# Optimization experiments

Hardware: AMD Instinct MI355X
Metric: run time of the kernel (lower is better)

## Reference

```python
import jax, jax.numpy as jnp
import numpy as np

N_NODE, N_USER = 100000, 30000
N_REL, N_BASIS = 8, 30
EMB, OUT = 32, 32
E = 1600000
BATCH = 16384
H1, H2, H3 = 64, 32, 16
NEG_SLOPE = 0.2


def setup_inputs() -> dict:
    key = jax.random.key(0)
    ks = jax.random.split(key, 20)
    g = lambda k, shape: jax.random.normal(k, shape, dtype=jnp.float32) * 0.05
    inp = {
        "x_ids": jnp.arange(N_NODE, dtype=jnp.int64 if jax.config.jax_enable_x64 else jnp.int32),
        "edge_index": jax.random.randint(ks[0], (2, E), 0, N_NODE),
        "edge_type": jax.random.randint(ks[1], (E,), 0, N_REL),
        "users": jax.random.randint(ks[2], (BATCH,), 0, N_USER),
        "bundles": jax.random.randint(ks[3], (BATCH,), 0, N_NODE),
        # parameters
        "emb": g(ks[4], (N_NODE, EMB)),
        "basis": g(ks[5], (N_BASIS, EMB, OUT)),
        "weight": g(ks[6], (N_REL, N_BASIS)),
        "att": g(ks[7], (N_REL, 2 * OUT)),
        "root": g(ks[8], (EMB, OUT)),
        "bias": jnp.zeros((OUT,), jnp.float32),
        "W1": g(ks[9], (2 * OUT, H1)), "b1": jnp.zeros((H1,), jnp.float32),
        "W2": g(ks[10], (H1, H2)), "b2": jnp.zeros((H2,), jnp.float32),
        "W3": g(ks[11], (H2, H3)), "b3": jnp.zeros((H3,), jnp.float32),
        "Wo": g(ks[12], (H3, 1)), "bo": jnp.zeros((1,), jnp.float32),
    }
    return inp


def _tgcn_fwd(x_ids, edge_index, edge_type, users, bundles,
              emb, basis, weight, att, root, bias,
              W1, b1, W2, b2, W3, b3, Wo, bo):
    N = emb.shape[0]
    R = weight.shape[0]
    O = basis.shape[2]
    x = emb[x_ids]                                   # (N, F) embedding lookup
    # basis decomposition: (R, F, O)
    w = (weight @ basis.reshape(N_BASIS, -1)).reshape(R, EMB, O)
    # transform every node under every relation once, then gather per edge
    xh = jnp.einsum('nf,rfo->nro', x, w)             # (N, R, O)
    src, dst = edge_index[0], edge_index[1]          # j (source), i (target)
    h_i = xh[dst, edge_type]                         # (E, O)
    h_j = xh[src, edge_type]                         # (E, O)
    a = att[edge_type]                               # (E, 2O)
    alpha = (h_i * a[:, :O]).sum(-1) + (h_j * a[:, O:]).sum(-1)
    alpha = jax.nn.leaky_relu(alpha, NEG_SLOPE)
    # segment softmax keyed by (target node, relation)
    seg_key = dst * R + edge_type
    n_seg = N * R
    amax = jax.ops.segment_max(alpha, seg_key, num_segments=n_seg)
    ex = jnp.exp(alpha - amax[seg_key])
    denom = jax.ops.segment_sum(ex, seg_key, num_segments=n_seg)
    alpha = ex / (denom[seg_key] + 1e-16)
    # scatter-add weighted messages into target nodes
    agg = jax.ops.segment_sum(h_j * alpha[:, None], dst, num_segments=N)
    h = jax.nn.relu(agg + x @ root + bias)           # update + ReLU
    z = jnp.concatenate([h[users], h[bundles]], axis=1)  # (B, 2O)
    z = jax.nn.relu(z @ W1 + b1)
    z = jax.nn.relu(z @ W2 + b2)
    z = jax.nn.relu(z @ W3 + b3)
    return z @ Wo + bo                               # (B, 1) logits


def reference(x_ids, edge_index, edge_type, users, bundles,
              emb, basis, weight, att, root, bias,
              W1, b1, W2, b2, W3, b3, Wo, bo):
    return _tgcn_fwd(x_ids, edge_index, edge_type, users, bundles,
                     emb, basis, weight, att, root, bias,
                     W1, b1, W2, b2, W3, b3, Wo, bo)
```

## Files before the change

### kernel.cpp

```cpp
#include <hip/hip_runtime.h>
#include <hip/hip_bf16.h>

#define N_NODE 100000
#define N_REL  8
#define EMB    32
#define OUT    32
#define N_BASIS 30
#define E_EDGE 1600000
#define BATCH  16384
#define H1 64
#define H2 32
#define H3 16
#define NEG_SLOPE 0.2f

#define BSH   8
#define NBKT  391
#define BCAP  5120
#define PCH   2048

#define K5T   128

#define NPB   16
#define K1GRID 2048


__global__ __launch_bounds__(256) void k0f(const float* __restrict__ weight,
                                           const float* __restrict__ basis,
                                           const float* __restrict__ att,
                                           float* __restrict__ w,
                                           float* __restrict__ wa,
                                           unsigned* __restrict__ bcnt) {
    __shared__ float wl[N_REL * EMB * OUT];
    int t = threadIdx.x;
    for (int i = t; i < N_REL * EMB * OUT; i += 256) {
        int r = i >> 10, fo = i & 1023;
        float acc = 0.f;
        #pragma unroll
        for (int b = 0; b < N_BASIS; b++)
            acc = fmaf(weight[r * N_BASIS + b], basis[b * (EMB * OUT) + fo], acc);
        wl[i] = acc;
        w[i] = acc;
    }
    __syncthreads();
    for (int i = t; i < 512; i += 256) {
        int which = i >> 8, rf = i & 255, r = rf >> 5, f = rf & 31;
        const float* wrow = wl + (r * 32 + f) * 32;
        const float* arow = att + r * 64 + which * 32;
        float acc = 0.f;
        #pragma unroll
        for (int o = 0; o < 32; o++) acc = fmaf(wrow[o], arow[o], acc);
        wa[i] = acc;
    }
    for (int i = t; i < NBKT; i += 256) bcnt[i] = 0;
}

__global__ __launch_bounds__(256) void k1x(const float* __restrict__ emb,
                                           const float* __restrict__ w,
                                           const float* __restrict__ att,
                                           const float* __restrict__ root,
                                           const float* __restrict__ bias,
                                           unsigned short* __restrict__ xh,
                                           float* __restrict__ p_i,
                                           float* __restrict__ p_j,
                                           float* __restrict__ agg) {
    __shared__ float xs[2][NPB * EMB];
    __shared__ float atts[N_REL * 2 * OUT];
    __shared__ float rootsT[OUT * 34];
    __shared__ float biass[OUT];

    const int t = threadIdx.x;
    const int o = t & 31;
    const int r = t >> 5;

    float wc[EMB];
    #pragma unroll
    for (int f = 0; f < EMB; f++) wc[f] = w[(r * EMB + f) * OUT + o];
    #pragma unroll
    for (int f = 0; f < EMB; f++) asm volatile("" : "+v"(wc[f]));

    for (int i = t; i < 512; i += 256) atts[i] = att[i];
    for (int i = t; i < EMB * OUT; i += 256) {
        int f = i >> 5, oo = i & 31;
        rootsT[oo * 34 + f] = root[i];
    }
    if (t < OUT) biass[t] = bias[t];

    int n0 = blockIdx.x * NPB;
    ((float2*)xs[0])[t] = ((const float2*)(emb + (size_t)n0 * EMB))[t];
    __syncthreads();

    const float aco = atts[r * 64 + o];
    const float acj = atts[r * 64 + 32 + o];

    int buf = 0;
    for (; n0 < N_NODE; n0 += K1GRID * NPB) {
        int n1 = n0 + K1GRID * NPB;
        if (n1 < N_NODE)
            ((float2*)xs[buf ^ 1])[t] = ((const float2*)(emb + (size_t)n1 * EMB))[t];

        #pragma unroll 4
        for (int k = 0; k < NPB; k++) {
            const float4* xr = (const float4*)&xs[buf][k * EMB];
            float a = 0.f;
            #pragma unroll
            for (int c = 0; c < 8; c++) {
                float4 xv = xr[c];
                a = fmaf(xv.x, wc[4 * c + 0], a);
                a = fmaf(xv.y, wc[4 * c + 1], a);
                a = fmaf(xv.z, wc[4 * c + 2], a);
                a = fmaf(xv.w, wc[4 * c + 3], a);
            }
            __hip_bfloat16 hb = __float2bfloat16(a);
            xh[(size_t)(n0 + k) * 256 + t] = *(unsigned short*)&hb;

            float ai = a * aco, aj = a * acj;
            #pragma unroll
            for (int m = 1; m <= 16; m <<= 1) {
                ai += __shfl_xor(ai, m, 64);
                aj += __shfl_xor(aj, m, 64);
            }
            if (o == 0)      p_i[(n0 + k) * N_REL + r] = ai;
            else if (o == 1) p_j[(n0 + k) * N_REL + r] = aj;

            if (r == (k & 7)) {
                float g = biass[o];
                const float* rt = &rootsT[o * 34];
                #pragma unroll
                for (int c = 0; c < 8; c++) {
                    float4 xv = xr[c];
                    float2 r0 = *(const float2*)&rt[4 * c];
                    float2 r1 = *(const float2*)&rt[4 * c + 2];
                    g = fmaf(xv.x, r0.x, g); g = fmaf(xv.y, r0.y, g);
                    g = fmaf(xv.z, r1.x, g); g = fmaf(xv.w, r1.y, g);
                }
                agg[(size_t)(n0 + k) * OUT + o] = g;
            }
        }
        __syncthreads();
        buf ^= 1;
    }
}

__global__ __launch_bounds__(256) void k_part(const int* __restrict__ src,
                                              const int* __restrict__ dst,
                                              const int* __restrict__ et,
                                              unsigned* __restrict__ bcnt,
                                              unsigned* __restrict__ part) {
    __shared__ unsigned long long stage[PCH];
    __shared__ unsigned hist[NBKT], lbase[NBKT], lcur[NBKT], gbase[NBKT];
    __shared__ unsigned sc[256];
    int t = threadIdx.x;
    for (int i = t; i < NBKT; i += 256) hist[i] = 0;
    __syncthreads();
    int beg = blockIdx.x * PCH, end = min(beg + PCH, E_EDGE);
    int n = end - beg;
    int ng = n >> 2;
    int g0 = t, g1 = t + 256;
    bool has0 = g0 < ng, has1 = g1 < ng;
    int4 s0v = {}, d0v = {}, e0v = {}, s1v = {}, d1v = {}, e1v = {};
    if (has0) {
        s0v = *(const int4*)&src[beg + 4 * g0];
        d0v = *(const int4*)&dst[beg + 4 * g0];
        e0v = *(const int4*)&et[beg + 4 * g0];
    }
    if (has1) {
        s1v = *(const int4*)&src[beg + 4 * g1];
        d1v = *(const int4*)&dst[beg + 4 * g1];
        e1v = *(const int4*)&et[beg + 4 * g1];
    }
    if (has0) {
        atomicAdd(&hist[(unsigned)d0v.x >> BSH], 1u);
        atomicAdd(&hist[(unsigned)d0v.y >> BSH], 1u);
        atomicAdd(&hist[(unsigned)d0v.z >> BSH], 1u);
        atomicAdd(&hist[(unsigned)d0v.w >> BSH], 1u);
    }
    if (has1) {
        atomicAdd(&hist[(unsigned)d1v.x >> BSH], 1u);
        atomicAdd(&hist[(unsigned)d1v.y >> BSH], 1u);
        atomicAdd(&hist[(unsigned)d1v.z >> BSH], 1u);
        atomicAdd(&hist[(unsigned)d1v.w >> BSH], 1u);
    }
    __syncthreads();
    unsigned v0 = (2 * t < NBKT) ? hist[2 * t] : 0u;
    unsigned v1 = (2 * t + 1 < NBKT) ? hist[2 * t + 1] : 0u;
    unsigned s = v0 + v1;
    sc[t] = s;
    __syncthreads();
    for (int off = 1; off < 256; off <<= 1) {
        unsigned y = (t >= off) ? sc[t - off] : 0u;
        __syncthreads();
        sc[t] += y;
        __syncthreads();
    }
    unsigned ex = sc[t] - s;
    if (2 * t < NBKT)     { lbase[2 * t] = ex;          lcur[2 * t] = ex; }
    if (2 * t + 1 < NBKT) { lbase[2 * t + 1] = ex + v0; lcur[2 * t + 1] = ex + v0; }
    __syncthreads();
    #define K_PART_STAGE(dd, ss, ee) do {                                   \
        unsigned b_ = (unsigned)(dd) >> BSH;                                \
        unsigned ent_ = ((unsigned)((dd) & 255) << 20)                      \
                      | ((unsigned)(ss) << 3) | (unsigned)(ee);             \
        unsigned pos_ = atomicAdd(&lcur[b_], 1u);                           \
        stage[pos_] = ((unsigned long long)b_ << 32) | ent_; } while (0)
    if (has0) {
        K_PART_STAGE(d0v.x, s0v.x, e0v.x);
        K_PART_STAGE(d0v.y, s0v.y, e0v.y);
        K_PART_STAGE(d0v.z, s0v.z, e0v.z);
        K_PART_STAGE(d0v.w, s0v.w, e0v.w);
    }
    if (has1) {
        K_PART_STAGE(d1v.x, s1v.x, e1v.x);
        K_PART_STAGE(d1v.y, s1v.y, e1v.y);
        K_PART_STAGE(d1v.z, s1v.z, e1v.z);
        K_PART_STAGE(d1v.w, s1v.w, e1v.w);
    }
    #undef K_PART_STAGE
    __syncthreads();
    for (int i = t; i < NBKT; i += 256)
        if (hist[i]) gbase[i] = atomicAdd(&bcnt[i], hist[i]);
    __syncthreads();
    for (int i = t; i < n; i += 256) {
        unsigned long long s64 = stage[i];
        unsigned b = (unsigned)(s64 >> 32);
        unsigned ent = (unsigned)s64;
        part[b * BCAP + gbase[b] + (i - lbase[b])] = ent;
    }
}

__global__ __launch_bounds__(256) void k_sort(const unsigned* __restrict__ bcnt,
                                              const unsigned* __restrict__ part,
                                              int* __restrict__ payload,
                                              int* __restrict__ begp,
                                              int* __restrict__ endp) {
    __shared__ unsigned ent[BCAP];
    __shared__ unsigned ent2[BCAP];
    __shared__ unsigned hist[256], dbase[256], dcur[256];
    __shared__ unsigned sc[256];
    int t = threadIdx.x;
    int b = blockIdx.x;
    unsigned s0 = (unsigned)b * BCAP;
    int n = (int)bcnt[b];
    if (n > BCAP) n = BCAP;
    hist[t] = 0;
    __syncthreads();
    int n4 = n & ~3;
    for (int i = 4 * t; i < n4; i += 1024) {
        uint4 e4 = *(const uint4*)&part[s0 + i];
        ent[i + 0] = e4.x; atomicAdd(&hist[e4.x >> 20], 1u);
        ent[i + 1] = e4.y; atomicAdd(&hist[e4.y >> 20], 1u);
        ent[i + 2] = e4.z; atomicAdd(&hist[e4.z >> 20], 1u);
        ent[i + 3] = e4.w; atomicAdd(&hist[e4.w >> 20], 1u);
    }
    for (int i = n4 + t; i < n; i += 256) {
        unsigned e = part[s0 + i];
        ent[i] = e;
        atomicAdd(&hist[e >> 20], 1u);
    }
    __syncthreads();
    unsigned v = hist[t];
    sc[t] = v;
    __syncthreads();
    for (int off = 1; off < 256; off <<= 1) {
        unsigned y = (t >= off) ? sc[t - off] : 0u;
        __syncthreads();
        sc[t] += y;
        __syncthreads();
    }
    unsigned ex = sc[t] - v;
    dbase[t] = ex;
    dcur[t] = ex;
    __syncthreads();
    int d = (b << BSH) + t;
    if (d < N_NODE) {
        begp[d] = (int)(s0 + dbase[t]);
        endp[d] = (int)(s0 + dbase[t] + hist[t]);
    }
    for (int i = t; i < n; i += 256) {
        unsigned e = ent[i];
        unsigned pos = atomicAdd(&dcur[e >> 20], 1u);
        ent2[pos] = e & 0xFFFFFu;
    }
    __syncthreads();
    for (int i = 4 * t; i < n4; i += 1024) {
        uint4 o4 = { ent2[i + 0], ent2[i + 1], ent2[i + 2], ent2[i + 3] };
        *(uint4*)&payload[s0 + i] = o4;
    }
    for (int i = n4 + t; i < n; i += 256) payload[s0 + i] = (int)ent2[i];
}

__global__ __launch_bounds__(256) void k_agg(const int* __restrict__ begp,
                                             const int* __restrict__ endp,
                                             const int* __restrict__ payload,
                                             const float* __restrict__ p_i,
                                             const float* __restrict__ p_j,
                                             const unsigned short* __restrict__ xh,
                                             float* __restrict__ agg,
                                             int d0, int d1) {
    int d = d0 + blockIdx.x * 4 + (threadIdx.x >> 6);
    if (d >= d1) return;
    const int lane = threadIdx.x & 63;
    const int h = lane >> 5;
    const int o = lane & 31;
    const int beg = begp[d], end = endp[d];
    const int cnt = end - beg;
    if (cnt == 0) return;

    float pid[8];
    #pragma unroll
    for (int k = 0; k < 8; k++) pid[k] = p_i[(d << 3) | k];

    if (cnt <= 64) {
        int sr = 0, r = 0; float ev = 0.f;
        if (lane < cnt) {
            sr = payload[beg + lane];
            r = sr & 7;
            float pi = pid[0];
            #pragma unroll
            for (int k = 1; k < 8; k++) pi = (r == k) ? pid[k] : pi;
            float a = pi + p_j[sr];
            a = (a >= 0.f) ? a : NEG_SLOPE * a;
            ev = __expf(a);
        }
        float sex[8];
        #pragma unroll
        for (int k = 0; k < 8; k++) sex[k] = (r == k) ? ev : 0.f;
        #pragma unroll
        for (int k = 0; k < 8; k++) {
            #pragma unroll
            for (int m = 1; m <= 32; m <<= 1) sex[k] += __shfl_xor(sex[k], m, 64);
        }
        float de = sex[0];
        #pragma unroll
        for (int k = 1; k < 8; k++) de = (r == k) ? sex[k] : de;
        float al = ev / (de + 1e-16f);

        float w0 = 0.f, w1 = 0.f, w2 = 0.f, w3 = 0.f;
        for (int j0 = 0; j0 < cnt; j0 += 8) {
            float b0 = __shfl(al, j0 + h,     64);
            float b1 = __shfl(al, j0 + 2 + h, 64);
            float b2 = __shfl(al, j0 + 4 + h, 64);
            float b3 = __shfl(al, j0 + 6 + h, 64);
            int t0 = payload[beg + j0 + h]     & 0xFFFFF;
            int t1 = payload[beg + j0 + 2 + h] & 0xFFFFF;
            int t2 = payload[beg + j0 + 4 + h] & 0xFFFFF;
            int t3 = payload[beg + j0 + 6 + h] & 0xFFFFF;
            float x0 = __uint_as_float((unsigned)xh[((unsigned)t0 << 5) + o] << 16);
            float x1 = __uint_as_float((unsigned)xh[((unsigned)t1 << 5) + o] << 16);
            float x2 = __uint_as_float((unsigned)xh[((unsigned)t2 << 5) + o] << 16);
            float x3 = __uint_as_float((unsigned)xh[((unsigned)t3 << 5) + o] << 16);
            w0 = fmaf(b0, x0, w0); w1 = fmaf(b1, x1, w1);
            w2 = fmaf(b2, x2, w2); w3 = fmaf(b3, x3, w3);
        }
        float vv = (w0 + w1) + (w2 + w3);
        vv += __shfl_xor(vv, 32, 64);
        if (h == 0) agg[(size_t)d * OUT + o] += vv;
        return;
    }

    float sex[8] = {0.f,0.f,0.f,0.f,0.f,0.f,0.f,0.f};
    for (int i = beg + lane; i < end; i += 64) {
        int sr = payload[i];
        int r = sr & 7;
        float pi = pid[0];
        #pragma unroll
        for (int k = 1; k < 8; k++) pi = (r == k) ? pid[k] : pi;
        float a = pi + p_j[sr];
        a = (a >= 0.f) ? a : NEG_SLOPE * a;
        float ev = __expf(a);
        #pragma unroll
        for (int k = 0; k < 8; k++) sex[k] += (r == k) ? ev : 0.f;
    }
    #pragma unroll
    for (int k = 0; k < 8; k++) {
        #pragma unroll
        for (int m = 1; m <= 32; m <<= 1) sex[k] += __shfl_xor(sex[k], m, 64);
    }
    float v0 = 0.f;
    for (int c = beg; c < end; c += 64) {
        int i = c + lane;
        int sr = 0; float al = 0.f;
        if (i < end) {
            sr = payload[i];
            int r = sr & 7;
            float pi = pid[0];
            #pragma unroll
            for (int k = 1; k < 8; k++) pi = (r == k) ? pid[k] : pi;
            float a = pi + p_j[sr];
            a = (a >= 0.f) ? a : NEG_SLOPE * a;
            float ev = __expf(a);
            float de = sex[0];
            #pragma unroll
            for (int k = 1; k < 8; k++) de = (r == k) ? sex[k] : de;
            al = ev / (de + 1e-16f);
        }
        int m = min(64, end - c);
        for (int j0 = 0; j0 < m; j0 += 2) {
            int e0 = j0 + h;
            float a0 = __shfl(al, e0, 64); int s0 = __shfl(sr, e0, 64);
            if (e0 < m) {
                float xv = __uint_as_float((unsigned)xh[((unsigned)s0 << 5) + o] << 16);
                v0 = fmaf(a0, xv, v0);
            }
        }
    }
    float vv = v0;
    vv += __shfl_xor(vv, 32, 64);
    if (h == 0) agg[(size_t)d * OUT + o] += vv;
}

__global__ __launch_bounds__(K5T, 1) void k5_mlp(const int* __restrict__ users,
                                                 const int* __restrict__ bundles,
                                                 const float* __restrict__ agg,
                                                 const float* __restrict__ W1,
                                                 const float* __restrict__ b1,
                                                 const float* __restrict__ W2,
                                                 const float* __restrict__ b2,
                                                 const float* __restrict__ W3,
                                                 const float* __restrict__ b3,
                                                 const float* __restrict__ Wo,
                                                 const float* __restrict__ bo,
                                                 float* __restrict__ out) {
    __shared__ float4 W1s[2 * OUT * H1 / 4];
    __shared__ float4 W2s[H1 * H2 / 4];
    __shared__ float4 W3s[H2 * H3 / 4];
    __shared__ float b1s[H1], b2s[H2], b3s[H3], Wos[H3];
    __shared__ float bos;
    __shared__ float zs[K5T * 65];
    __shared__ float h1s[K5T * 65];
    const int t = threadIdx.x;

    const float4* W14 = (const float4*)W1;
    const float4* W24 = (const float4*)W2;
    const float4* W34 = (const float4*)W3;
    for (int i = t; i < 1024; i += K5T) W1s[i] = W14[i];
    for (int i = t; i < 512; i += K5T) W2s[i] = W24[i];
    for (int i = t; i < 128; i += K5T) W3s[i] = W34[i];
    if (t < H1) b1s[t] = b1[t];
    if (t < H2) b2s[t] = b2[t];
    if (t < H3) { b3s[t] = b3[t]; Wos[t] = Wo[t]; }
    if (t == 0) bos = bo[0];

    const int item = blockIdx.x * K5T + t;
    const int u = users[item], v = bundles[item];
    const float4* av = (const float4*)agg;
    float* zrow = &zs[t * 65];
    float* h1row = &h1s[t * 65];

    #pragma unroll
    for (int c = 0; c < 8; c++) {
        float4 x = av[(size_t)u * 8 + c];
        zrow[4 * c + 0] = fmaxf(x.x, 0.f); zrow[4 * c + 1] = fmaxf(x.y, 0.f);
        zrow[4 * c + 2] = fmaxf(x.z, 0.f); zrow[4 * c + 3] = fmaxf(x.w, 0.f);
    }
    #pragma unroll
    for (int c = 0; c < 8; c++) {
        float4 x = av[(size_t)v * 8 + c];
        zrow[32 + 4 * c + 0] = fmaxf(x.x, 0.f); zrow[32 + 4 * c + 1] = fmaxf(x.y, 0.f);
        zrow[32 + 4 * c + 2] = fmaxf(x.z, 0.f); zrow[32 + 4 * c + 3] = fmaxf(x.w, 0.f);
    }
    __syncthreads();

    #pragma unroll 4
    for (int j4 = 0; j4 < 16; j4++) {
        float a0 = b1s[4 * j4 + 0], a1 = b1s[4 * j4 + 1];
        float a2 = b1s[4 * j4 + 2], a3 = b1s[4 * j4 + 3];
        #pragma unroll 16
        for (int k = 0; k < 2 * OUT; k++) {
            float zk = zrow[k];
            float4 wv = W1s[k * 16 + j4];
            a0 = fmaf(zk, wv.x, a0); a1 = fmaf(zk, wv.y, a1);
            a2 = fmaf(zk, wv.z, a2); a3 = fmaf(zk, wv.w, a3);
        }
        h1row[4 * j4 + 0] = fmaxf(a0, 0.f); h1row[4 * j4 + 1] = fmaxf(a1, 0.f);
        h1row[4 * j4 + 2] = fmaxf(a2, 0.f); h1row[4 * j4 + 3] = fmaxf(a3, 0.f);
    }

    #pragma unroll 4
    for (int j4 = 0; j4 < 8; j4++) {
        float a0 = b2s[4 * j4 + 0], a1 = b2s[4 * j4 + 1];
        float a2 = b2s[4 * j4 + 2], a3 = b2s[4 * j4 + 3];
        #pragma unroll 16
        for (int k = 0; k < H1; k++) {
            float hk = h1row[k];
            float4 wv = W2s[k * 8 + j4];
            a0 = fmaf(hk, wv.x, a0); a1 = fmaf(hk, wv.y, a1);
            a2 = fmaf(hk, wv.z, a2); a3 = fmaf(hk, wv.w, a3);
        }
        zrow[4 * j4 + 0] = fmaxf(a0, 0.f); zrow[4 * j4 + 1] = fmaxf(a1, 0.f);
        zrow[4 * j4 + 2] = fmaxf(a2, 0.f); zrow[4 * j4 + 3] = fmaxf(a3, 0.f);
    }

    float h3v[16];
    #pragma unroll
    for (int j4 = 0; j4 < 4; j4++) {
        float a0 = b3s[4 * j4 + 0], a1 = b3s[4 * j4 + 1];
        float a2 = b3s[4 * j4 + 2], a3 = b3s[4 * j4 + 3];
        #pragma unroll 16
        for (int k = 0; k < H2; k++) {
            float hk = zrow[k];
            float4 wv = W3s[k * 4 + j4];
            a0 = fmaf(hk, wv.x, a0); a1 = fmaf(hk, wv.y, a1);
            a2 = fmaf(hk, wv.z, a2); a3 = fmaf(hk, wv.w, a3);
        }
        h3v[4 * j4 + 0] = fmaxf(a0, 0.f); h3v[4 * j4 + 1] = fmaxf(a1, 0.f);
        h3v[4 * j4 + 2] = fmaxf(a2, 0.f); h3v[4 * j4 + 3] = fmaxf(a3, 0.f);
    }

    float acc = bos;
    #pragma unroll
    for (int k = 0; k < H3; k++) acc = fmaf(h3v[k], Wos[k], acc);
    out[item] = acc;
}

extern "C" void kernel_launch(void* const* d_in, const int* in_sizes, int n_in,
                              void* d_out, int out_size, void* d_ws, size_t ws_size,
                              hipStream_t stream) {
    (void)in_sizes; (void)n_in; (void)out_size; (void)ws_size;
    const int*   eidx   = (const int*)d_in[1];
    const int*   etype  = (const int*)d_in[2];
    const int*   users  = (const int*)d_in[3];
    const int*   bund   = (const int*)d_in[4];
    const float* emb    = (const float*)d_in[5];
    const float* basis  = (const float*)d_in[6];
    const float* weight = (const float*)d_in[7];
    const float* att    = (const float*)d_in[8];
    const float* root   = (const float*)d_in[9];
    const float* bias   = (const float*)d_in[10];
    const float* W1 = (const float*)d_in[11]; const float* b1 = (const float*)d_in[12];
    const float* W2 = (const float*)d_in[13]; const float* b2 = (const float*)d_in[14];
    const float* W3 = (const float*)d_in[15]; const float* b3 = (const float*)d_in[16];
    const float* Wo = (const float*)d_in[17]; const float* bo = (const float*)d_in[18];
    float* out = (float*)d_out;

    const int* src = eidx;
    const int* dst = eidx + E_EDGE;

    float* ws       = (float*)d_ws;
    float* w        = ws;
    float* wa       = w + N_REL * EMB * OUT;
    unsigned short* xh = (unsigned short*)(wa + 512);
    float* p_i      = (float*)(xh + (size_t)N_NODE * 256);
    float* p_j      = p_i + N_NODE * N_REL;
    float* agg      = p_j + N_NODE * N_REL;
    int*   payload  = (int*)(agg + (long)N_NODE * OUT);
    int*   begp     = payload + NBKT * BCAP;
    int*   endp     = begp + N_NODE;
    unsigned* bcnt  = (unsigned*)(endp + N_NODE);
    unsigned* part  = (unsigned*)agg;

    k0f<<<1, 256, 0, stream>>>(weight, basis, att, w, wa, bcnt);
    k_part<<<(E_EDGE + PCH - 1) / PCH, 256, 0, stream>>>(src, dst, etype, bcnt, part);
    k_sort<<<NBKT, 256, 0, stream>>>(bcnt, part, payload, begp, endp);
    k1x<<<K1GRID, 256, 0, stream>>>(emb, w, att, root, bias, xh, p_i, p_j, agg);
    k_agg<<<12500, 256, 0, stream>>>(begp, endp, payload, p_i, p_j, xh, agg,
                                     0, 50000);
    k_agg<<<12500, 256, 0, stream>>>(begp, endp, payload, p_i, p_j, xh, agg,
                                     50000, 100000);
    k5_mlp<<<BATCH / K5T, K5T, 0, stream>>>(users, bund, agg, W1, b1, W2, b2, W3, b3,
                                            Wo, bo, out);
}
```

Measured before the change: 349.4 us.

## Restructure node transform kernel: precomputed attention projections, one tile per block

The node-transform kernel now computes attention logit partials p_i/p_j straight from embeddings using the precomputed W·att vectors (wa), instead of reducing the transformed features with warp shuffles. Each block handles a fixed 32-node tile with no grid-stride loop or double buffering. Each thread holds weights for two relations so it produces two outputs per node, and the root transform is split into its own dense phase over all threads. The aim is to remove shuffle reductions and idle-lane branches, at the cost of more registers per thread and no overlap of embedding loads with compute.

Result: faster. 317.4 us (-9.1%).

```diff
diff --git a/kernel.cpp b/kernel.cpp
--- a/kernel.cpp
+++ b/kernel.cpp
@@ -20,8 +20,9 @@
 
 #define K5T   128
 
-#define NPB   16
-#define K1GRID 2048
+#define NPB   32
+#define K1GRID (N_NODE / NPB)
+#define RTS   36
 
 
 __global__ __launch_bounds__(256) void k0f(const float* __restrict__ weight,
@@ -56,88 +57,120 @@
 
 __global__ __launch_bounds__(256) void k1x(const float* __restrict__ emb,
                                            const float* __restrict__ w,
-                                           const float* __restrict__ att,
+                                           const float* __restrict__ wa,
                                            const float* __restrict__ root,
                                            const float* __restrict__ bias,
                                            unsigned short* __restrict__ xh,
                                            float* __restrict__ p_i,
                                            float* __restrict__ p_j,
                                            float* __restrict__ agg) {
-    __shared__ float xs[2][NPB * EMB];
-    __shared__ float atts[N_REL * 2 * OUT];
-    __shared__ float rootsT[OUT * 34];
+    __shared__ float xs[NPB * EMB];
+    __shared__ float rootsT[OUT * RTS];
+    __shared__ float was[16 * RTS];
     __shared__ float biass[OUT];
 
     const int t = threadIdx.x;
-    const int o = t & 31;
-    const int r = t >> 5;
-
-    float wc[EMB];
-    #pragma unroll
-    for (int f = 0; f < EMB; f++) wc[f] = w[(r * EMB + f) * OUT + o];
-    #pragma unroll
-    for (int f = 0; f < EMB; f++) asm volatile("" : "+v"(wc[f]));
-
-    for (int i = t; i < 512; i += 256) atts[i] = att[i];
+    const int n0 = blockIdx.x * NPB;
+
+    const int ro = t & 127;
+    const int rhi = ro >> 5, olo = ro & 31;
+    float wc0[EMB], wc1[EMB];
+    #pragma unroll
+    for (int f = 0; f < EMB; f++) {
+        wc0[f] = w[rhi * 1024 + f * 32 + olo];
+        wc1[f] = w[rhi * 1024 + 4096 + f * 32 + olo];
+    }
+    #pragma unroll
+    for (int f = 0; f < EMB; f++) asm volatile("" : "+v"(wc0[f]), "+v"(wc1[f]));
+
+    ((float4*)xs)[t] = ((const float4*)(emb + (size_t)n0 * EMB))[t];
     for (int i = t; i < EMB * OUT; i += 256) {
         int f = i >> 5, oo = i & 31;
-        rootsT[oo * 34 + f] = root[i];
+        rootsT[oo * RTS + f] = root[i];
+    }
+    for (int i = t; i < 512; i += 256) {
+        int which = i >> 8, r = (i >> 5) & 7, f = i & 31;
+        was[(which * 8 + r) * RTS + f] = wa[i];
     }
     if (t < OUT) biass[t] = bias[t];
-
-    int n0 = blockIdx.x * NPB;
-    ((float2*)xs[0])[t] = ((const float2*)(emb + (size_t)n0 * EMB))[t];
-    __syncthreads();
-
-    const float aco = atts[r * 64 + o];
-    const float acj = atts[r * 64 + 32 + o];
-
-    int buf = 0;
-    for (; n0 < N_NODE; n0 += K1GRID * NPB) {
-        int n1 = n0 + K1GRID * NPB;
-        if (n1 < N_NODE)
-            ((float2*)xs[buf ^ 1])[t] = ((const float2*)(emb + (size_t)n1 * EMB))[t];
-
+    __syncthreads();
+
+    {
+        const int n = t >> 3, r = t & 7;
+        const float4* xr = (const float4*)&xs[n * EMB];
+        const float4* wi = (const float4*)&was[r * RTS];
+        const float4* wj = (const float4*)&was[(8 + r) * RTS];
+        float ai = 0.f, aj = 0.f;
+        #pragma unroll
+        for (int c = 0; c < 8; c++) {
+            float4 xv = xr[c];
+            float4 vi = wi[c], vj = wj[c];
+            ai = fmaf(xv.x, vi.x, ai); ai = fmaf(xv.y, vi.y, ai);
+            ai = fmaf(xv.z, vi.z, ai); ai = fmaf(xv.w, vi.w, ai);
+            aj = fmaf(xv.x, vj.x, aj); aj = fmaf(xv.y, vj.y, aj);
+            aj = fmaf(xv.z, vj.z, aj); aj = fmaf(xv.w, vj.w, aj);
+        }
+        p_i[n0 * N_REL + t] = ai;
+        p_j[n0 * N_REL + t] = aj;
+    }
+
+    {
+        const int o = t & 31, ng = t >> 5;
+        const float4* rt = (const float4*)&rootsT[o * RTS];
+        float4 r0 = rt[0], r1 = rt[1], r2 = rt[2], r3 = rt[3];
+        float4 r4 = rt[4], r5 = rt[5], r6 = rt[6], r7 = rt[7];
+        float bv = biass[o];
+        #pragma unroll
+        for (int q = 0; q < 4; q++) {
+            int n = ng * 4 + q;
+            const float4* xr = (const float4*)&xs[n * EMB];
+            float g = bv;
+            float4 xv;
+            xv = xr[0]; g = fmaf(xv.x, r0.x, g); g = fmaf(xv.y, r0.y, g);
+                        g = fmaf(xv.z, r0.z, g); g = fmaf(xv.w, r0.w, g);
+            xv = xr[1]; g = fmaf(xv.x, r1.x, g); g = fmaf(xv.y, r1.y, g);
+                        g = fmaf(xv.z, r1.z, g); g = fmaf(xv.w, r1.w, g);
+            xv = xr[2]; g = fmaf(xv.x, r2.x, g); g = fmaf(xv.y, r2.y, g);
+                        g = fmaf(xv.z, r2.z, g); g = fmaf(xv.w, r2.w, g);
+            xv = xr[3]; g = fmaf(xv.x, r3.x, g); g = fmaf(xv.y, r3.y, g);
+                        g = fmaf(xv.z, r3.z, g); g = fmaf(xv.w, r3.w, g);
+            xv = xr[4]; g = fmaf(xv.x, r4.x, g); g = fmaf(xv.y, r4.y, g);
+                        g = fmaf(xv.z, r4.z, g); g = fmaf(xv.w, r4.w, g);
+            xv = xr[5]; g = fmaf(xv.x, r5.x, g); g = fmaf(xv.y, r5.y, g);
+                        g = fmaf(xv.z, r5.z, g); g = fmaf(xv.w, r5.w, g);
+            xv = xr[6]; g = fmaf(xv.x, r6.x, g); g = fmaf(xv.y, r6.y, g);
+                        g = fmaf(xv.z, r6.z, g); g = fmaf(xv.w, r6.w, g);
+            xv = xr[7]; g = fmaf(xv.x, r7.x, g); g = fmaf(xv.y, r7.y, g);
+                        g = fmaf(xv.z, r7.z, g); g = fmaf(xv.w, r7.w, g);
+            agg[(size_t)(n0 + n) * OUT + o] = g;
+        }
+    }
+
+    {
+        const int half = t >> 7;
         #pragma unroll 4
-        for (int k = 0; k < NPB; k++) {
-            const float4* xr = (const float4*)&xs[buf][k * EMB];
-            float a = 0.f;
+        for (int s = 0; s < 16; s++) {
+            int n = 2 * s + half;
+            const float4* xr = (const float4*)&xs[n * EMB];
+            float a0 = 0.f, a1 = 0.f;
             #pragma unroll
             for (int c = 0; c < 8; c++) {
                 float4 xv = xr[c];
-                a = fmaf(xv.x, wc[4 * c + 0], a);
-                a = fmaf(xv.y, wc[4 * c + 1], a);
-                a = fmaf(xv.z, wc[4 * c + 2], a);
-                a = fmaf(xv.w, wc[4 * c + 3], a);
+                a0 = fmaf(xv.x, wc0[4 * c + 0], a0);
+                a0 = fmaf(xv.y, wc0[4 * c + 1], a0);
+                a0 = fmaf(xv.z, wc0[4 * c + 2], a0);
+                a0 = fmaf(xv.w, wc0[4 * c + 3], a0);
+                a1 = fmaf(xv.x, wc1[4 * c + 0], a1);
+                a1 = fmaf(xv.y, wc1[4 * c + 1], a1);
+                a1 = fmaf(xv.z, wc1[4 * c + 2], a1);
+                a1 = fmaf(xv.w, wc1[4 * c + 3], a1);
             }
-            __hip_bfloat16 hb = __float2bfloat16(a);
-            xh[(size_t)(n0 + k) * 256 + t] = *(unsigned short*)&hb;
-
-            float ai = a * aco, aj = a * acj;
-            #pragma unroll
-            for (int m = 1; m <= 16; m <<= 1) {
-                ai += __shfl_xor(ai, m, 64);
-                aj += __shfl_xor(aj, m, 64);
-            }
-            if (o == 0)      p_i[(n0 + k) * N_REL + r] = ai;
-            else if (o == 1) p_j[(n0 + k) * N_REL + r] = aj;
-
-            if (r == (k & 7)) {
-                float g = biass[o];
-                const float* rt = &rootsT[o * 34];
-                #pragma unroll
-                for (int c = 0; c < 8; c++) {
-                    float4 xv = xr[c];
-                    float2 r0 = *(const float2*)&rt[4 * c];
-                    float2 r1 = *(const float2*)&rt[4 * c + 2];
-                    g = fmaf(xv.x, r0.x, g); g = fmaf(xv.y, r0.y, g);
-                    g = fmaf(xv.z, r1.x, g); g = fmaf(xv.w, r1.y, g);
-                }
-                agg[(size_t)(n0 + k) * OUT + o] = g;
-            }
-        }
-        __syncthreads();
-        buf ^= 1;
+            __hip_bfloat16 b0 = __float2bfloat16(a0);
+            __hip_bfloat16 b1 = __float2bfloat16(a1);
+            unsigned short* xp = xh + (size_t)(n0 + n) * 256;
+            xp[ro]       = *(unsigned short*)&b0;
+            xp[ro + 128] = *(unsigned short*)&b1;
+        }
     }
 }
 
@@ -551,7 +584,7 @@
     k0f<<<1, 256, 0, stream>>>(weight, basis, att, w, wa, bcnt);
     k_part<<<(E_EDGE + PCH - 1) / PCH, 256, 0, stream>>>(src, dst, etype, bcnt, part);
     k_sort<<<NBKT, 256, 0, stream>>>(bcnt, part, payload, begp, endp);
-    k1x<<<K1GRID, 256, 0, stream>>>(emb, w, att, root, bias, xh, p_i, p_j, agg);
+    k1x<<<K1GRID, 256, 0, stream>>>(emb, w, wa, root, bias, xh, p_i, p_j, agg);
     k_agg<<<12500, 256, 0, stream>>>(begp, endp, payload, p_i, p_j, xh, agg,
                                      0, 50000);
     k_agg<<<12500, 256, 0, stream>>>(begp, endp, payload, p_i, p_j, xh, agg,
```
